# Kernel tuning notes

Hardware: AMD Instinct MI355X
Metric: run time of the kernel (lower is better)

## Reference

```python
import jax, jax.numpy as jnp
import numpy as np


def lrelu(x):
    return jnp.where(x > 0, x, 0.1 * x)


def setup_inputs() -> dict:
    key = jax.random.key(0)
    ks = jax.random.split(key, 16)
    L, B, E = 160, 16, 512
    C, H, DM, DO = 256, 512, 128, 512  # conv channels, enc_hid, d_mlp, dec_hid

    def rn(k, shape, scale=0.05):
        return jax.random.normal(k, shape, dtype=jnp.float32) * scale

    return {
        "x": rn(ks[0], (L, B, E), 1.0),
        "h": rn(ks[1], (B, H), 1.0),
        "conv_w": rn(ks[2], (C, E, 3)),
        "conv_b": rn(ks[3], (C,)),
        "bn_g": jnp.ones((C,), jnp.float32),
        "bn_b": jnp.zeros((C,), jnp.float32),
        "W1": rn(ks[4], (DM, 2 * (C + 2) + H)),
        "b1": rn(ks[5], (DM,)),
        "W2": rn(ks[6], (DM, DM)), "b2": rn(ks[7], (DM,)),
        "W3": rn(ks[8], (DM, DM)), "b3": rn(ks[9], (DM,)),
        "W4": rn(ks[10], (DM, DM)), "b4": rn(ks[11], (DM,)),
        "W5": rn(ks[12], (DM, DM)), "b5": rn(ks[13], (DM,)),
        "W6": rn(ks[14], (DO, DM)), "b6": rn(ks[15], (DO,)),
    }


def reference(x, h, conv_w, conv_b, bn_g, bn_b,
              W1, b1, W2, b2, W3, b3, W4, b4, W5, b5, W6, b6):
    L, B, E = x.shape
    # --- ConvLayer: Conv1d(k=3, pad=1) -> LeakyReLU(0.1) -> BatchNorm1d (training stats)
    xc = jnp.transpose(x, (1, 2, 0))  # (B, E, L)
    y = jax.lax.conv_general_dilated(xc, conv_w, (1,), [(1, 1)],
                                     dimension_numbers=("NCH", "OIH", "NCH"))
    y = lrelu(y + conv_b[None, :, None])
    mu = y.mean(axis=(0, 2), keepdims=True)
    var = y.var(axis=(0, 2), keepdims=True)  # biased variance (torch training BN)
    y = (y - mu) * jax.lax.rsqrt(var + 1e-5)
    y = y * bn_g[None, :, None] + bn_b[None, :, None]
    y = jnp.transpose(y, (0, 2, 1))  # (B, L, C)

    # --- coordinate features: [(i/sqrt(L)-2)/2, (i % sqrt(L) - 2)/2]
    sL = np.sqrt(L)
    i = jnp.arange(L, dtype=jnp.float32)
    coords = jnp.stack([(i / sL - 2.0) / 2.0, (jnp.mod(i, sL) - 2.0) / 2.0], axis=-1)  # (L, 2)
    xf = jnp.concatenate([y, jnp.broadcast_to(coords[None], (B, L, 2))], axis=-1)  # (B, L, C+2)
    Cp = xf.shape[-1]

    # --- g_mlp first Linear decomposed over [x_i | x_j | h] feature blocks:
    # x_i[b,a,c] = xf[b,c] (varies with dim2); x_j[b,a,c] = cat(xf[b,a], h[b]) (varies with dim1)
    W1i = W1[:, :Cp]            # acts on x_i
    W1jx = W1[:, Cp:2 * Cp]     # acts on x part of x_j
    W1jh = W1[:, 2 * Cp:]       # acts on h part of x_j
    u = jnp.einsum('blc,dc->bld', xf, W1i)                     # (B, L, DM), index = dim2
    v = jnp.einsum('blc,dc->bld', xf, W1jx) + (h @ W1jh.T)[:, None, :]  # (B, L, DM), index = dim1
    z = lrelu(v[:, :, None, :] + u[:, None, :, :] + b1)        # (B, L, L, DM)
    z = lrelu(z @ W2.T + b2)
    z = lrelu(z @ W3.T + b3)
    z = lrelu(z @ W4.T + b4)
    s = z.sum(axis=(1, 2))  # sum over all L*L pairs -> (B, DM)

    # --- f_mlp
    s = lrelu(s @ W5.T + b5)
    return lrelu(s @ W6.T + b6)  # (B, dec_hid)
```

## Files before the change

kernel.cpp:

```cpp
#include <hip/hip_runtime.h>
#include <cstdint>

typedef unsigned short u16;
typedef uint32_t u32;

typedef __bf16 bf16x8 __attribute__((ext_vector_type(8)));
typedef float  f32x2  __attribute__((ext_vector_type(2)));
typedef float  f32x4  __attribute__((ext_vector_type(4)));
typedef float  f32x16 __attribute__((ext_vector_type(16)));
typedef u16    u16x4  __attribute__((ext_vector_type(4)));
typedef u16    u16x8  __attribute__((ext_vector_type(8)));

__device__ __forceinline__ u16 f2bf(float f) {
    u32 x = __float_as_uint(f);
    return (u16)((x + 0x7FFFu + ((x >> 16) & 1u)) >> 16);
}
__device__ __forceinline__ float lrelu(float x) { return fmaxf(x, 0.1f * x); }

__device__ __forceinline__ u32 pack_rn(float lo, float hi) {
    u32 a = __float_as_uint(lo) + 0x8000u;
    u32 b = __float_as_uint(hi) + 0x8000u;
    return __builtin_amdgcn_perm(b, a, 0x07060302u);
}

__global__ __launch_bounds__(256) void k_prep(
    const float* __restrict__ x, const float* __restrict__ conv_w,
    const float* __restrict__ W2, const float* __restrict__ W3, const float* __restrict__ W4,
    const float* __restrict__ b2, const float* __restrict__ b3, const float* __restrict__ b4,
    const float* __restrict__ h, const float* __restrict__ W1,
    u16* __restrict__ xb, u16* __restrict__ wcb_f, u16* __restrict__ wfrag,
    u16* __restrict__ w1frag, float* __restrict__ hW, float* __restrict__ zero0)
{
    int blk = blockIdx.x, tid = threadIdx.x;
    if (blk < 1280) {
        int o = (blk * 256 + tid) * 4;
        int e = o & 511;
        int bl = o >> 9;
        int b = bl / 160, l = bl % 160;
        f32x4 v = *(const f32x4*)(x + ((size_t)(l * 16 + b)) * 512 + e);
        u16x4 ov;
        ov[0] = f2bf(v[0]); ov[1] = f2bf(v[1]); ov[2] = f2bf(v[2]); ov[3] = f2bf(v[3]);
        *(u16x4*)&xb[o] = ov;
    } else if (blk < 1472) {
        int g = (blk - 1280) * 256 + tid;
        int lane = g & 63;
        int ks = (g >> 6) % 48;
        int cb = g / 3072;
        int c = cb * 16 + (lane & 15);
        int quad = lane >> 4;
        int k0 = ks * 32 + quad * 8;
        int tap = k0 >> 9, e0 = k0 & 511;
        u16x8 ov;
        #pragma unroll
        for (int j = 0; j < 8; j++)
            ov[j] = f2bf(conv_w[((size_t)c * 512 + e0 + j) * 3 + tap]);
        *(u16x8*)&wcb_f[(size_t)g * 8] = ov;
    } else if (blk < 1526) {
        int o = ((blk - 1472) * 256 + tid) * 4;
        int layer = o / 18432, rem = o % 18432;
        int ks9 = rem >> 11;
        int rem2 = rem & 2047;
        int hh = rem2 >> 10;
        int rem3 = rem2 & 1023;
        int n = rem3 >> 3, j0 = rem3 & 7;
        const float* W = (layer == 0) ? W2 : (layer == 1) ? W3 : W4;
        const float* bi = (layer == 0) ? b2 : (layer == 1) ? b3 : b4;
        u16x4 ov;
        if (ks9 < 8) {
            f32x4 v = *(const f32x4*)(W + (size_t)n * 128 + 16 * ks9 + 8 * hh + j0);
            ov[0] = f2bf(v[0]); ov[1] = f2bf(v[1]); ov[2] = f2bf(v[2]); ov[3] = f2bf(v[3]);
        } else {
            ov[0] = (hh == 0 && j0 == 0) ? f2bf(bi[n]) : (u16)0;
            ov[1] = 0; ov[2] = 0; ov[3] = 0;
        }
        *(u16x4*)&wfrag[o] = ov;
    } else if (blk < 1598) {
        int o = ((blk - 1526) * 256 + tid) * 4;
        int nt = o / 4608;
        int rem = o % 4608;
        int ks = rem >> 9;
        int rem2 = rem & 511;
        int lane = rem2 >> 3, j0 = rem2 & 7;
        int n = nt * 16 + (lane & 15);
        int k0 = ks * 32 + (lane >> 4) * 8 + j0;
        const float* wr = (n < 128) ? (W1 + (size_t)n * 1028)
                                    : (W1 + (size_t)(n - 128) * 1028 + 258);
        u16x4 ov;
        #pragma unroll
        for (int q = 0; q < 4; q++) {
            int k = k0 + q;
            ov[q] = (k < 258) ? f2bf(wr[k]) : (u16)0;
        }
        *(u16x4*)&w1frag[o] = ov;
    } else if (blk < 1726) {
        int gid = (blk - 1598) * 256 + tid;
        int outp = gid >> 4, q = gid & 15;
        int b = outp >> 7, d = outp & 127;
        const float* hr = h + (size_t)b * 512;
        const float* wr = W1 + (size_t)d * 1028 + 516;
        float acc = 0.f;
        #pragma unroll
        for (int c = 0; c < 8; c++) {
            int k = c * 64 + q * 4;
            f32x4 hv = *(const f32x4*)(hr + k);
            f32x4 wv = *(const f32x4*)(wr + k);
            acc += hv[0]*wv[0] + hv[1]*wv[1] + hv[2]*wv[2] + hv[3]*wv[3];
        }
        acc += __shfl_xor(acc, 1); acc += __shfl_xor(acc, 2);
        acc += __shfl_xor(acc, 4); acc += __shfl_xor(acc, 8);
        if (q == 0) hW[outp] = acc;
    } else {
        int idx = (blk - 1726) * 256 + tid;
        if (idx < 640) {
            f32x4 z = {0.f, 0.f, 0.f, 0.f};
            *(f32x4*)&zero0[idx * 4] = z;
        }
    }
}

__global__ __launch_bounds__(256, 4) void k_conv(
    const u16* __restrict__ xb, const u16* __restrict__ wcb_f,
    const float* __restrict__ conv_b,
    float* __restrict__ ws_y, float* __restrict__ stats)
{
    __shared__ u16 xs[18 * 520];
    int tid = threadIdx.x, wg = blockIdx.x;
    int rowtile = wg >> 2, cg = wg & 3;
    int b = rowtile / 10, l0 = (rowtile % 10) * 16;

    for (int t = tid; t < 18 * 64; t += 256) {
        int s = t >> 6, ch = t & 63;
        int lg = l0 + s - 1;
        u16x8 v = {};
        if (lg >= 0 && lg < 160)
            v = *(const u16x8*)(xb + ((size_t)(b * 160 + lg)) * 512 + ch * 8);
        *(u16x8*)&xs[s * 520 + ch * 8] = v;
    }
    __syncthreads();

    int lane = tid & 63, w = tid >> 6;
    int row16 = lane & 15, quad = lane >> 4;
    int cb = cg * 4 + w;
    int c_n = cb * 16 + row16;
    const u16* wb = wcb_f + (size_t)cb * 24576;

    f32x4 acc0 = {0,0,0,0};
    for (int ks4 = 0; ks4 < 48; ks4 += 4) {
        bf16x8 wf[4];
        #pragma unroll
        for (int q = 0; q < 4; q++)
            wf[q] = *(const bf16x8*)(wb + (size_t)((ks4 + q) * 64 + lane) * 8);
        #pragma unroll
        for (int q = 0; q < 4; q++) {
            int k = (ks4 + q) * 32 + quad * 8;
            int tap = k >> 9, e = k & 511;
            bf16x8 a0 = *(const bf16x8*)&xs[(row16 + tap) * 520 + e];
            acc0 = __builtin_amdgcn_mfma_f32_16x16x32_bf16(a0, wf[q], acc0, 0, 0, 0);
        }
    }

    float bias = conv_b[c_n];
    float sum = 0.f, sq = 0.f;
    #pragma unroll
    for (int r = 0; r < 4; r++) {
        float v = lrelu(acc0[r] + bias);
        int lr = l0 + quad * 4 + r;
        ws_y[((size_t)(b * 160 + lr)) * 256 + c_n] = v;
        sum += v; sq += v * v;
    }
    sum += __shfl_xor(sum, 16); sum += __shfl_xor(sum, 32);
    sq  += __shfl_xor(sq, 16);  sq  += __shfl_xor(sq, 32);
    if (quad == 0) {
        atomicAdd(&stats[c_n], sum);
        atomicAdd(&stats[256 + c_n], sq);
    }
}

__global__ __launch_bounds__(256) void k_uv(
    const float* __restrict__ ws_y, const float* __restrict__ stats,
    const float* __restrict__ bn_g, const float* __restrict__ bn_b,
    const u16* __restrict__ w1frag, const float* __restrict__ b1,
    const float* __restrict__ hW,
    float* __restrict__ uu, float* __restrict__ vv)
{
    __shared__ float a_s[256], c_s[256];
    __shared__ __align__(16) u16 xfs[16 * 296];
    int tid = threadIdx.x;
    int row0 = blockIdx.x * 16;
    int b = row0 / 160, l0 = row0 % 160;
    {
        int c = tid;
        float mu  = stats[c] * (1.0f / 2560.0f);
        float var = stats[256 + c] * (1.0f / 2560.0f) - mu * mu;
        float rs  = rsqrtf(var + 1e-5f) * bn_g[c];
        a_s[c] = rs;
        c_s[c] = bn_b[c] - mu * rs;
    }
    __syncthreads();
    float sLf = sqrtf(160.0f);
    for (int idx = tid; idx < 16 * 288; idx += 256) {
        int r = idx / 288, c = idx - r * 288;
        int l = l0 + r;
        float v = 0.f;
        if (c < 256) {
            v = ws_y[((size_t)(b * 160 + l)) * 256 + c] * a_s[c] + c_s[c];
        } else if (c == 256) {
            v = ((float)l / sLf - 2.0f) * 0.5f;
        } else if (c == 257) {
            float fi = (float)l;
            float m = fi - floorf(fi / sLf) * sLf;
            v = (m - 2.0f) * 0.5f;
        }
        xfs[r * 296 + c] = f2bf(v);
    }
    __syncthreads();

    int lane = tid & 63, w = tid >> 6;
    int row16 = lane & 15, quad = lane >> 4;

    bf16x8 af[9];
    #pragma unroll
    for (int ks = 0; ks < 9; ks++)
        af[ks] = *(const bf16x8*)&xfs[row16 * 296 + ks * 32 + quad * 8];

    f32x4 acc[4];
    #pragma unroll
    for (int nt = 0; nt < 4; nt++) {
        f32x4 a = {0.f, 0.f, 0.f, 0.f};
        #pragma unroll
        for (int ks = 0; ks < 9; ks++) {
            bf16x8 bf = *(const bf16x8*)(w1frag +
                (size_t)(((w * 4 + nt) * 9 + ks) * 64 + lane) * 8);
            a = __builtin_amdgcn_mfma_f32_16x16x32_bf16(af[ks], bf, a, 0, 0, 0);
        }
        acc[nt] = a;
    }

    #pragma unroll
    for (int nt = 0; nt < 4; nt++) {
        int n = (w * 4 + nt) * 16 + row16;
        bool isv = n >= 128;
        int d = n & 127;
        float add = isv ? (hW[b * 128 + d] + b1[d]) : 0.f;
        float* dst = isv ? vv : uu;
        #pragma unroll
        for (int r = 0; r < 4; r++) {
            int l = l0 + quad * 4 + r;
            dst[((size_t)(b * 160 + l)) * 128 + d] = acc[nt][r] + add;
        }
    }
}

__global__ __launch_bounds__(256, 4) void k_mlp(
    const float* __restrict__ vv, const float* __restrict__ uu,
    const u16* __restrict__ wfrag,
    float* __restrict__ s_glob)
{
    __shared__ __align__(16) u16 Wlds[18432];
    __shared__ float spart[128];
    int tid = threadIdx.x;
    int wave = tid >> 6, lane = tid & 63;
    int h = lane >> 5, lo = lane & 31;
    int b = blockIdx.x / 200, sub = blockIdx.x % 200;
    int tileb = sub * 4 + wave;

    if (tid < 128) spart[tid] = 0.f;

    u32 selv = h ? 0x07060302u : 0x05040100u;
    uint4 biasfrag;
    biasfrag.x = (h == 0) ? 0x00003F80u : 0u;
    biasfrag.y = 0u; biasfrag.z = 0u; biasfrag.w = 0u;

    f32x16 Z;
    #pragma unroll
    for (int r = 0; r < 16; r++) Z[r] = 0.f;

    uint4 B[8], Bn[8];
    float ssum[4];

    int i  = (tileb / 10) * 2  + (lo >> 4);
    int jj = (tileb % 10) * 16 + (lo & 15);
    const float* vr = vv + ((size_t)(b * 160 + i))  * 128 + 8 * h;
    const float* ur = uu + ((size_t)(b * 160 + jj)) * 128 + 8 * h;

    for (int layer = 0; layer < 3; layer++) {
        __syncthreads();
        {
            const uint4* src = (const uint4*)(wfrag + layer * 18432);
            #pragma unroll
            for (int it = 0; it < 9; it++) {
                int idx = it * 256 + tid;
                *(uint4*)&Wlds[idx * 8] = src[idx];
            }
        }
        __syncthreads();

        if (layer == 0) {
            #pragma unroll
            for (int ks = 0; ks < 8; ks++) {
                f32x4 v0 = *(const f32x4*)(vr + 16 * ks);
                f32x4 v1 = *(const f32x4*)(vr + 16 * ks + 4);
                f32x4 u0 = *(const f32x4*)(ur + 16 * ks);
                f32x4 u1 = *(const f32x4*)(ur + 16 * ks + 4);
                uint4 d;
                d.x = pack_rn(lrelu(v0[0]+u0[0]), lrelu(v0[1]+u0[1]));
                d.y = pack_rn(lrelu(v0[2]+u0[2]), lrelu(v0[3]+u0[3]));
                d.z = pack_rn(lrelu(v1[0]+u1[0]), lrelu(v1[1]+u1[1]));
                d.w = pack_rn(lrelu(v1[2]+u1[2]), lrelu(v1[3]+u1[3]));
                B[ks] = d;
            }
        }

        #pragma unroll
        for (int nt = 0; nt < 4; nt++) {
            f32x16 a;
            #pragma unroll
            for (int ks = 0; ks < 9; ks++) {
                bf16x8 wf = *(const bf16x8*)&Wlds[(size_t)(ks * 256 + h * 128 + nt * 32 + lo) * 8];
                uint4 zu = (ks < 8) ? B[ks] : biasfrag;
                bf16x8 zf = *(bf16x8*)&zu;
                if (layer < 2)
                    a = __builtin_amdgcn_mfma_f32_32x32x16_bf16(wf, zf, ks ? a : Z, 0, 0, 0);
                else
                    a = __builtin_amdgcn_mfma_f32_32x32x16_bf16(zf, wf, ks ? a : Z, 0, 0, 0);
            }

            if (layer < 2) {
                u32 own[4][2], oth[4][2];
                #pragma unroll
                for (int c = 0; c < 4; c++)
                    #pragma unroll
                    for (int p = 0; p < 2; p++)
                        own[c][p] = pack_rn(lrelu(a[c + 8*p]),
                                            lrelu(a[c + 4 + 8*p]));
                #pragma unroll
                for (int c = 0; c < 4; c++)
                    #pragma unroll
                    for (int p = 0; p < 2; p++)
                        oth[c][p] = (u32)__shfl_xor((int)own[c][p], 32);
                #pragma unroll
                for (int p = 0; p < 2; p++) {
                    u32 dA0 = __builtin_amdgcn_perm(own[1][p], own[0][p], selv);
                    u32 dB0 = __builtin_amdgcn_perm(oth[1][p], oth[0][p], selv);
                    u32 dA1 = __builtin_amdgcn_perm(own[3][p], own[2][p], selv);
                    u32 dB1 = __builtin_amdgcn_perm(oth[3][p], oth[2][p], selv);
                    uint4 d;
                    d.x = h ? dB0 : dA0;
                    d.y = h ? dB1 : dA1;
                    d.z = h ? dA0 : dB0;
                    d.w = h ? dA1 : dB1;
                    Bn[2 * nt + p] = d;
                }
            } else {
                float t = 0.f;
                #pragma unroll
                for (int r = 0; r < 16; r++)
                    t += lrelu(a[r]);
                ssum[nt] = t;
            }
        }

        if (layer < 2) {
            #pragma unroll
            for (int ks = 0; ks < 8; ks++) B[ks] = Bn[ks];
        }
    }

    #pragma unroll
    for (int nt = 0; nt < 4; nt++) {
        float v = ssum[nt] + __shfl_xor(ssum[nt], 32);
        if (h == 0) atomicAdd(&spart[nt * 32 + lo], v);
    }
    __syncthreads();
    if (tid < 128) atomicAdd(&s_glob[b * 128 + tid], spart[tid]);
}

__global__ __launch_bounds__(256) void k_final(
    const float* __restrict__ s_glob,
    const float* __restrict__ W5, const float* __restrict__ b5,
    const float* __restrict__ W6, const float* __restrict__ b6,
    float* __restrict__ out)
{
    __shared__ float sh[128], t5[128];
    int b = blockIdx.x, tid = threadIdx.x;
    if (tid < 128) sh[tid] = s_glob[b * 128 + tid];
    __syncthreads();
    if (tid < 128) {
        const float* wr = W5 + (size_t)tid * 128;
        float acc = b5[tid];
        #pragma unroll
        for (int k = 0; k < 128; k += 4) {
            f32x4 wv = *(const f32x4*)(wr + k);
            f32x4 sv = *(const f32x4*)&sh[k];
            acc += wv[0]*sv[0] + wv[1]*sv[1] + wv[2]*sv[2] + wv[3]*sv[3];
        }
        t5[tid] = lrelu(acc);
    }
    __syncthreads();
    #pragma unroll
    for (int q = 0; q < 2; q++) {
        int o = q * 256 + tid;
        const float* wr = W6 + (size_t)o * 128;
        float acc = b6[o];
        #pragma unroll
        for (int k = 0; k < 128; k += 4) {
            f32x4 wv = *(const f32x4*)(wr + k);
            f32x4 tv = *(const f32x4*)&t5[k];
            acc += wv[0]*tv[0] + wv[1]*tv[1] + wv[2]*tv[2] + wv[3]*tv[3];
        }
        out[b * 512 + o] = lrelu(acc);
    }
}

extern "C" void kernel_launch(void* const* d_in, const int* in_sizes, int n_in,
                              void* d_out, int out_size, void* d_ws, size_t ws_size,
                              hipStream_t stream)
{
    const float* x      = (const float*)d_in[0];
    const float* h      = (const float*)d_in[1];
    const float* conv_w = (const float*)d_in[2];
    const float* conv_b = (const float*)d_in[3];
    const float* bn_g   = (const float*)d_in[4];
    const float* bn_b   = (const float*)d_in[5];
    const float* W1     = (const float*)d_in[6];
    const float* b1     = (const float*)d_in[7];
    const float* W2     = (const float*)d_in[8];
    const float* b2     = (const float*)d_in[9];
    const float* W3     = (const float*)d_in[10];
    const float* b3     = (const float*)d_in[11];
    const float* W4     = (const float*)d_in[12];
    const float* b4     = (const float*)d_in[13];
    const float* W5     = (const float*)d_in[14];
    const float* b5     = (const float*)d_in[15];
    const float* W6     = (const float*)d_in[16];
    const float* b6     = (const float*)d_in[17];

    char* ws = (char*)d_ws;
    float* s_glob = (float*)(ws + 0);
    float* stats  = (float*)(ws + 8192);
    float* hW     = (float*)(ws + 10240);
    float* ws_y   = (float*)(ws + 18432);
    float* vv     = (float*)(ws + 2639872);
    float* uu     = (float*)(ws + 3950592);
    u16*   xb     = (u16*)  (ws + 5261312);
    u16*   wcb_f  = (u16*)  (ws + 7882752);
    u16*   wfrag  = (u16*)  (ws + 8669184);
    u16*   w1frag = (u16*)  (ws + 8779776);

    k_prep <<<1729, 256, 0, stream>>>(x, conv_w, W2, W3, W4, b2, b3, b4, h, W1,
                                      xb, wcb_f, wfrag, w1frag, hW, s_glob);
    k_conv <<<640, 256, 0, stream>>>(xb, wcb_f, conv_b, ws_y, stats);
    k_uv   <<<160, 256, 0, stream>>>(ws_y, stats, bn_g, bn_b, w1frag, b1, hW, uu, vv);
    k_mlp  <<<3200, 256, 0, stream>>>(vv, uu, wfrag, s_glob);
    k_final<<<16, 256, 0, stream>>>(s_glob, W5, b5, W6, b6, (float*)d_out);
}
```

Baseline: 193.2 us.

## Fuse all stages into one cooperative persistent kernel with grid syncs

Replaces the five separate launches with a single cooperative kernel that loops over each stage's work units and separates stages with grid-wide syncs, keeping a multi-launch fallback. This removes per-launch overhead and inter-kernel gaps. In exchange the grid is capped at occupancy × 256 CUs (max 800), so the 3200 MLP units run as a persistent loop. All stages now share one 37 KB LDS allocation and register budget, which may lower occupancy for the lighter stages, and the grid barriers add their own cost.

Measured after the change: 731.4 us. 279% more time.

```diff
diff --git a/kernel.cpp b/kernel.cpp
--- a/kernel.cpp
+++ b/kernel.cpp
@@ -1,5 +1,8 @@
 #include <hip/hip_runtime.h>
+#include <hip/hip_cooperative_groups.h>
 #include <cstdint>
+
+namespace cg = cooperative_groups;
 
 typedef unsigned short u16;
 typedef uint32_t u32;
@@ -23,15 +26,14 @@
     return __builtin_amdgcn_perm(b, a, 0x07060302u);
 }
 
-__global__ __launch_bounds__(256) void k_prep(
-    const float* __restrict__ x, const float* __restrict__ conv_w,
-    const float* __restrict__ W2, const float* __restrict__ W3, const float* __restrict__ W4,
-    const float* __restrict__ b2, const float* __restrict__ b3, const float* __restrict__ b4,
-    const float* __restrict__ h, const float* __restrict__ W1,
-    u16* __restrict__ xb, u16* __restrict__ wcb_f, u16* __restrict__ wfrag,
-    u16* __restrict__ w1frag, float* __restrict__ hW, float* __restrict__ zero0)
-{
-    int blk = blockIdx.x, tid = threadIdx.x;
+__device__ __forceinline__ void prep_block(int blk, int tid,
+    const float* x, const float* conv_w,
+    const float* W2, const float* W3, const float* W4,
+    const float* b2, const float* b3, const float* b4,
+    const float* h, const float* W1,
+    u16* xb, u16* wcb_f, u16* wfrag, u16* w1frag,
+    float* hW, float* zero0)
+{
     if (blk < 1280) {
         int o = (blk * 256 + tid) * 4;
         int e = o & 511;
@@ -118,14 +120,11 @@
     }
 }
 
-__global__ __launch_bounds__(256, 4) void k_conv(
-    const u16* __restrict__ xb, const u16* __restrict__ wcb_f,
-    const float* __restrict__ conv_b,
-    float* __restrict__ ws_y, float* __restrict__ stats)
-{
-    __shared__ u16 xs[18 * 520];
-    int tid = threadIdx.x, wg = blockIdx.x;
-    int rowtile = wg >> 2, cg = wg & 3;
+__device__ __forceinline__ void conv_block(int wg, int tid, u16* xs,
+    const u16* xb, const u16* wcb_f, const float* conv_b,
+    float* ws_y, float* stats)
+{
+    int rowtile = wg >> 2, cgp = wg & 3;
     int b = rowtile / 10, l0 = (rowtile % 10) * 16;
 
     for (int t = tid; t < 18 * 64; t += 256) {
@@ -140,7 +139,7 @@
 
     int lane = tid & 63, w = tid >> 6;
     int row16 = lane & 15, quad = lane >> 4;
-    int cb = cg * 4 + w;
+    int cb = cgp * 4 + w;
     int c_n = cb * 16 + row16;
     const u16* wb = wcb_f + (size_t)cb * 24576;
 
@@ -174,19 +173,19 @@
         atomicAdd(&stats[c_n], sum);
         atomicAdd(&stats[256 + c_n], sq);
     }
-}
-
-__global__ __launch_bounds__(256) void k_uv(
-    const float* __restrict__ ws_y, const float* __restrict__ stats,
-    const float* __restrict__ bn_g, const float* __restrict__ bn_b,
-    const u16* __restrict__ w1frag, const float* __restrict__ b1,
-    const float* __restrict__ hW,
-    float* __restrict__ uu, float* __restrict__ vv)
-{
-    __shared__ float a_s[256], c_s[256];
-    __shared__ __align__(16) u16 xfs[16 * 296];
-    int tid = threadIdx.x;
-    int row0 = blockIdx.x * 16;
+    __syncthreads();
+}
+
+__device__ __forceinline__ void uv_block(int wg, int tid, unsigned char* smem,
+    const float* ws_y, const float* stats,
+    const float* bn_g, const float* bn_b,
+    const u16* w1frag, const float* b1, const float* hW,
+    float* uu, float* vv)
+{
+    float* a_s = (float*)smem;
+    float* c_s = (float*)(smem + 1024);
+    u16*   xfs = (u16*)(smem + 2048);
+    int row0 = wg * 16;
     int b = row0 / 160, l0 = row0 % 160;
     {
         int c = tid;
@@ -223,7 +222,6 @@
     for (int ks = 0; ks < 9; ks++)
         af[ks] = *(const bf16x8*)&xfs[row16 * 296 + ks * 32 + quad * 8];
 
-    f32x4 acc[4];
     #pragma unroll
     for (int nt = 0; nt < 4; nt++) {
         f32x4 a = {0.f, 0.f, 0.f, 0.f};
@@ -233,11 +231,6 @@
                 (size_t)(((w * 4 + nt) * 9 + ks) * 64 + lane) * 8);
             a = __builtin_amdgcn_mfma_f32_16x16x32_bf16(af[ks], bf, a, 0, 0, 0);
         }
-        acc[nt] = a;
-    }
-
-    #pragma unroll
-    for (int nt = 0; nt < 4; nt++) {
         int n = (w * 4 + nt) * 16 + row16;
         bool isv = n >= 128;
         int d = n & 127;
@@ -246,22 +239,18 @@
         #pragma unroll
         for (int r = 0; r < 4; r++) {
             int l = l0 + quad * 4 + r;
-            dst[((size_t)(b * 160 + l)) * 128 + d] = acc[nt][r] + add;
-        }
-    }
-}
-
-__global__ __launch_bounds__(256, 4) void k_mlp(
-    const float* __restrict__ vv, const float* __restrict__ uu,
-    const u16* __restrict__ wfrag,
-    float* __restrict__ s_glob)
-{
-    __shared__ __align__(16) u16 Wlds[18432];
-    __shared__ float spart[128];
-    int tid = threadIdx.x;
+            dst[((size_t)(b * 160 + l)) * 128 + d] = a[r] + add;
+        }
+    }
+}
+
+__device__ __forceinline__ void mlp_unit(int unit, int tid,
+    u16* Wlds, float* spart,
+    const float* vv, const float* uu, const u16* wfrag, float* s_glob)
+{
     int wave = tid >> 6, lane = tid & 63;
     int h = lane >> 5, lo = lane & 31;
-    int b = blockIdx.x / 200, sub = blockIdx.x % 200;
+    int b = unit / 200, sub = unit % 200;
     int tileb = sub * 4 + wave;
 
     if (tid < 128) spart[tid] = 0.f;
@@ -375,14 +364,14 @@
     if (tid < 128) atomicAdd(&s_glob[b * 128 + tid], spart[tid]);
 }
 
-__global__ __launch_bounds__(256) void k_final(
-    const float* __restrict__ s_glob,
-    const float* __restrict__ W5, const float* __restrict__ b5,
-    const float* __restrict__ W6, const float* __restrict__ b6,
-    float* __restrict__ out)
-{
-    __shared__ float sh[128], t5[128];
-    int b = blockIdx.x, tid = threadIdx.x;
+__device__ __forceinline__ void final_block(int b, int tid, unsigned char* smem,
+    const float* s_glob,
+    const float* W5, const float* b5,
+    const float* W6, const float* b6,
+    float* out)
+{
+    float* sh = (float*)smem;
+    float* t5 = (float*)(smem + 512);
     if (tid < 128) sh[tid] = s_glob[b * 128 + tid];
     __syncthreads();
     if (tid < 128) {
@@ -410,6 +399,109 @@
         }
         out[b * 512 + o] = lrelu(acc);
     }
+}
+
+__global__ __launch_bounds__(256, 4) void k_all(
+    const float* __restrict__ x, const float* __restrict__ h,
+    const float* __restrict__ conv_w, const float* __restrict__ conv_b,
+    const float* __restrict__ bn_g, const float* __restrict__ bn_b,
+    const float* __restrict__ W1, const float* __restrict__ b1,
+    const float* __restrict__ W2, const float* __restrict__ b2,
+    const float* __restrict__ W3, const float* __restrict__ b3,
+    const float* __restrict__ W4, const float* __restrict__ b4,
+    const float* __restrict__ W5, const float* __restrict__ b5,
+    const float* __restrict__ W6, const float* __restrict__ b6,
+    float* __restrict__ out, char* __restrict__ ws)
+{
+    __shared__ __align__(16) unsigned char smem[37376];
+    int tid = threadIdx.x, wg = blockIdx.x, gdim = gridDim.x;
+    cg::grid_group grid = cg::this_grid();
+
+    float* s_glob = (float*)(ws);
+    float* stats  = (float*)(ws + 8192);
+    float* hW     = (float*)(ws + 10240);
+    float* ws_y   = (float*)(ws + 18432);
+    float* vv     = (float*)(ws + 2639872);
+    float* uu     = (float*)(ws + 3950592);
+    u16*   xb     = (u16*)  (ws + 5261312);
+    u16*   wcb_f  = (u16*)  (ws + 7882752);
+    u16*   wfrag  = (u16*)  (ws + 8669184);
+    u16*   w1frag = (u16*)  (ws + 8779776);
+
+    for (int g = wg; g < 1729; g += gdim)
+        prep_block(g, tid, x, conv_w, W2, W3, W4, b2, b3, b4, h, W1,
+                   xb, wcb_f, wfrag, w1frag, hW, s_glob);
+    __threadfence();
+    grid.sync();
+
+    for (int u = wg; u < 640; u += gdim)
+        conv_block(u, tid, (u16*)smem, xb, wcb_f, conv_b, ws_y, stats);
+    __threadfence();
+    grid.sync();
+
+    for (int u = wg; u < 160; u += gdim)
+        uv_block(u, tid, smem, ws_y, stats, bn_g, bn_b, w1frag, b1, hW, uu, vv);
+    __threadfence();
+    grid.sync();
+
+    {
+        u16*   Wlds  = (u16*)smem;
+        float* spart = (float*)(smem + 36864);
+        #pragma unroll 1
+        for (int u = wg; u < 3200; u += gdim)
+            mlp_unit(u, tid, Wlds, spart, vv, uu, wfrag, s_glob);
+    }
+    __threadfence();
+    grid.sync();
+
+    for (int u = wg; u < 16; u += gdim)
+        final_block(u, tid, smem, s_glob, W5, b5, W6, b6, out);
+}
+
+__global__ __launch_bounds__(256) void k_prep_g(
+    const float* x, const float* conv_w,
+    const float* W2, const float* W3, const float* W4,
+    const float* b2, const float* b3, const float* b4,
+    const float* h, const float* W1,
+    u16* xb, u16* wcb_f, u16* wfrag, u16* w1frag, float* hW, float* zero0)
+{
+    prep_block(blockIdx.x, threadIdx.x, x, conv_w, W2, W3, W4, b2, b3, b4,
+               h, W1, xb, wcb_f, wfrag, w1frag, hW, zero0);
+}
+
+__global__ __launch_bounds__(256, 4) void k_conv_g(
+    const u16* xb, const u16* wcb_f, const float* conv_b,
+    float* ws_y, float* stats)
+{
+    __shared__ u16 xs[18 * 520];
+    conv_block(blockIdx.x, threadIdx.x, xs, xb, wcb_f, conv_b, ws_y, stats);
+}
+
+__global__ __launch_bounds__(256) void k_uv_g(
+    const float* ws_y, const float* stats,
+    const float* bn_g, const float* bn_b,
+    const u16* w1frag, const float* b1, const float* hW,
+    float* uu, float* vv)
+{
+    __shared__ __align__(16) unsigned char smem[2048 + 16 * 296 * 2];
+    uv_block(blockIdx.x, threadIdx.x, smem, ws_y, stats, bn_g, bn_b,
+             w1frag, b1, hW, uu, vv);
+}
+
+__global__ __launch_bounds__(256, 4) void k_mlp_g(
+    const float* vv, const float* uu, const u16* wfrag, float* s_glob)
+{
+    __shared__ __align__(16) u16 Wlds[18432];
+    __shared__ float spart[128];
+    mlp_unit(blockIdx.x, threadIdx.x, Wlds, spart, vv, uu, wfrag, s_glob);
+}
+
+__global__ __launch_bounds__(256) void k_final_g(
+    const float* s_glob, const float* W5, const float* b5,
+    const float* W6, const float* b6, float* out)
+{
+    __shared__ __align__(16) unsigned char smem[1024];
+    final_block(blockIdx.x, threadIdx.x, smem, s_glob, W5, b5, W6, b6, out);
 }
 
 extern "C" void kernel_launch(void* const* d_in, const int* in_sizes, int n_in,
@@ -434,9 +526,10 @@
     const float* b5     = (const float*)d_in[15];
     const float* W6     = (const float*)d_in[16];
     const float* b6     = (const float*)d_in[17];
-
-    char* ws = (char*)d_ws;
-    float* s_glob = (float*)(ws + 0);
+    float* out = (float*)d_out;
+    char*  ws  = (char*)d_ws;
+
+    float* s_glob = (float*)(ws);
     float* stats  = (float*)(ws + 8192);
     float* hW     = (float*)(ws + 10240);
     float* ws_y   = (float*)(ws + 18432);
@@ -447,10 +540,31 @@
     u16*   wfrag  = (u16*)  (ws + 8669184);
     u16*   w1frag = (u16*)  (ws + 8779776);
 
-    k_prep <<<1729, 256, 0, stream>>>(x, conv_w, W2, W3, W4, b2, b3, b4, h, W1,
-                                      xb, wcb_f, wfrag, w1frag, hW, s_glob);
-    k_conv <<<640, 256, 0, stream>>>(xb, wcb_f, conv_b, ws_y, stats);
-    k_uv   <<<160, 256, 0, stream>>>(ws_y, stats, bn_g, bn_b, w1frag, b1, hW, uu, vv);
-    k_mlp  <<<3200, 256, 0, stream>>>(vv, uu, wfrag, s_glob);
-    k_final<<<16, 256, 0, stream>>>(s_glob, W5, b5, W6, b6, (float*)d_out);
-}
+    int occ = 0;
+    hipError_t qerr = hipOccupancyMaxActiveBlocksPerMultiprocessor(&occ, k_all, 256, 0);
+    int grid = (qerr == hipSuccess && occ > 0) ? occ * 256 : 0;
+    if (grid > 800) grid = 800;
+
+    bool done = false;
+    if (grid >= 256) {
+        void* params[] = {
+            (void*)&x, (void*)&h, (void*)&conv_w, (void*)&conv_b,
+            (void*)&bn_g, (void*)&bn_b, (void*)&W1, (void*)&b1,
+            (void*)&W2, (void*)&b2, (void*)&W3, (void*)&b3,
+            (void*)&W4, (void*)&b4, (void*)&W5, (void*)&b5,
+            (void*)&W6, (void*)&b6, (void*)&out, (void*)&ws
+        };
+        hipError_t lerr = hipLaunchCooperativeKernel(k_all, dim3(grid), dim3(256),
+                                                     params, 0, stream);
+        done = (lerr == hipSuccess);
+    }
+
+    if (!done) {
+        k_prep_g <<<1729, 256, 0, stream>>>(x, conv_w, W2, W3, W4, b2, b3, b4,
+                                            h, W1, xb, wcb_f, wfrag, w1frag, hW, s_glob);
+        k_conv_g <<<640, 256, 0, stream>>>(xb, wcb_f, conv_b, ws_y, stats);
+        k_uv_g   <<<160, 256, 0, stream>>>(ws_y, stats, bn_g, bn_b, w1frag, b1, hW, uu, vv);
+        k_mlp_g  <<<3200, 256, 0, stream>>>(vv, uu, wfrag, s_glob);
+        k_final_g<<<16, 256, 0, stream>>>(s_glob, W5, b5, W6, b6, out);
+    }
+}
```

## Fuse x bf16 conversion into conv load and final MLP into last mlp block

Applied to the files above, without the earlier changes.

The separate fp32-to-bf16 pass over x in the prep kernel is removed. The conv kernel now reads fp32 x directly and converts while filling shared memory, which drops one round trip through the workspace. The k_final launch is removed: the last k_mlp block, found through an atomic completion counter, computes the f_mlp for all 16 batches. This saves a launch, but the final stage now runs serially in a single block, and correctness depends on fences and the counter reset in k_prep.

Result: slower. 381.1 us (+97.3%).

```diff
diff --git a/kernel.cpp b/kernel.cpp
--- a/kernel.cpp
+++ b/kernel.cpp
@@ -5,7 +5,6 @@
 typedef uint32_t u32;
 
 typedef __bf16 bf16x8 __attribute__((ext_vector_type(8)));
-typedef float  f32x2  __attribute__((ext_vector_type(2)));
 typedef float  f32x4  __attribute__((ext_vector_type(4)));
 typedef float  f32x16 __attribute__((ext_vector_type(16)));
 typedef u16    u16x4  __attribute__((ext_vector_type(4)));
@@ -24,25 +23,16 @@
 }
 
 __global__ __launch_bounds__(256) void k_prep(
-    const float* __restrict__ x, const float* __restrict__ conv_w,
+    const float* __restrict__ conv_w,
     const float* __restrict__ W2, const float* __restrict__ W3, const float* __restrict__ W4,
     const float* __restrict__ b2, const float* __restrict__ b3, const float* __restrict__ b4,
     const float* __restrict__ h, const float* __restrict__ W1,
-    u16* __restrict__ xb, u16* __restrict__ wcb_f, u16* __restrict__ wfrag,
-    u16* __restrict__ w1frag, float* __restrict__ hW, float* __restrict__ zero0)
+    u16* __restrict__ wcb_f, u16* __restrict__ wfrag, u16* __restrict__ w1frag,
+    float* __restrict__ hW, float* __restrict__ zero0, u32* __restrict__ ctr)
 {
     int blk = blockIdx.x, tid = threadIdx.x;
-    if (blk < 1280) {
-        int o = (blk * 256 + tid) * 4;
-        int e = o & 511;
-        int bl = o >> 9;
-        int b = bl / 160, l = bl % 160;
-        f32x4 v = *(const f32x4*)(x + ((size_t)(l * 16 + b)) * 512 + e);
-        u16x4 ov;
-        ov[0] = f2bf(v[0]); ov[1] = f2bf(v[1]); ov[2] = f2bf(v[2]); ov[3] = f2bf(v[3]);
-        *(u16x4*)&xb[o] = ov;
-    } else if (blk < 1472) {
-        int g = (blk - 1280) * 256 + tid;
+    if (blk < 192) {
+        int g = blk * 256 + tid;
         int lane = g & 63;
         int ks = (g >> 6) % 48;
         int cb = g / 3072;
@@ -55,8 +45,8 @@
         for (int j = 0; j < 8; j++)
             ov[j] = f2bf(conv_w[((size_t)c * 512 + e0 + j) * 3 + tap]);
         *(u16x8*)&wcb_f[(size_t)g * 8] = ov;
-    } else if (blk < 1526) {
-        int o = ((blk - 1472) * 256 + tid) * 4;
+    } else if (blk < 246) {
+        int o = ((blk - 192) * 256 + tid) * 4;
         int layer = o / 18432, rem = o % 18432;
         int ks9 = rem >> 11;
         int rem2 = rem & 2047;
@@ -74,8 +64,8 @@
             ov[1] = 0; ov[2] = 0; ov[3] = 0;
         }
         *(u16x4*)&wfrag[o] = ov;
-    } else if (blk < 1598) {
-        int o = ((blk - 1526) * 256 + tid) * 4;
+    } else if (blk < 318) {
+        int o = ((blk - 246) * 256 + tid) * 4;
         int nt = o / 4608;
         int rem = o % 4608;
         int ks = rem >> 9;
@@ -92,8 +82,8 @@
             ov[q] = (k < 258) ? f2bf(wr[k]) : (u16)0;
         }
         *(u16x4*)&w1frag[o] = ov;
-    } else if (blk < 1726) {
-        int gid = (blk - 1598) * 256 + tid;
+    } else if (blk < 446) {
+        int gid = (blk - 318) * 256 + tid;
         int outp = gid >> 4, q = gid & 15;
         int b = outp >> 7, d = outp & 127;
         const float* hr = h + (size_t)b * 512;
@@ -110,37 +100,45 @@
         acc += __shfl_xor(acc, 4); acc += __shfl_xor(acc, 8);
         if (q == 0) hW[outp] = acc;
     } else {
-        int idx = (blk - 1726) * 256 + tid;
+        int idx = (blk - 446) * 256 + tid;
         if (idx < 640) {
             f32x4 z = {0.f, 0.f, 0.f, 0.f};
             *(f32x4*)&zero0[idx * 4] = z;
         }
+        if (idx == 0) *ctr = 0u;
     }
 }
 
 __global__ __launch_bounds__(256, 4) void k_conv(
-    const u16* __restrict__ xb, const u16* __restrict__ wcb_f,
+    const float* __restrict__ x, const u16* __restrict__ wcb_f,
     const float* __restrict__ conv_b,
     float* __restrict__ ws_y, float* __restrict__ stats)
 {
     __shared__ u16 xs[18 * 520];
     int tid = threadIdx.x, wg = blockIdx.x;
-    int rowtile = wg >> 2, cg = wg & 3;
+    int rowtile = wg >> 2, cgp = wg & 3;
     int b = rowtile / 10, l0 = (rowtile % 10) * 16;
 
     for (int t = tid; t < 18 * 64; t += 256) {
         int s = t >> 6, ch = t & 63;
         int lg = l0 + s - 1;
-        u16x8 v = {};
-        if (lg >= 0 && lg < 160)
-            v = *(const u16x8*)(xb + ((size_t)(b * 160 + lg)) * 512 + ch * 8);
-        *(u16x8*)&xs[s * 520 + ch * 8] = v;
+        u16x8 ov = {};
+        if (lg >= 0 && lg < 160) {
+            const float* src = x + ((size_t)(lg * 16 + b)) * 512 + ch * 8;
+            f32x4 v0 = *(const f32x4*)src;
+            f32x4 v1 = *(const f32x4*)(src + 4);
+            ov[0] = f2bf(v0[0]); ov[1] = f2bf(v0[1]);
+            ov[2] = f2bf(v0[2]); ov[3] = f2bf(v0[3]);
+            ov[4] = f2bf(v1[0]); ov[5] = f2bf(v1[1]);
+            ov[6] = f2bf(v1[2]); ov[7] = f2bf(v1[3]);
+        }
+        *(u16x8*)&xs[s * 520 + ch * 8] = ov;
     }
     __syncthreads();
 
     int lane = tid & 63, w = tid >> 6;
     int row16 = lane & 15, quad = lane >> 4;
-    int cb = cg * 4 + w;
+    int cb = cgp * 4 + w;
     int c_n = cb * 16 + row16;
     const u16* wb = wcb_f + (size_t)cb * 24576;
 
@@ -223,7 +221,6 @@
     for (int ks = 0; ks < 9; ks++)
         af[ks] = *(const bf16x8*)&xfs[row16 * 296 + ks * 32 + quad * 8];
 
-    f32x4 acc[4];
     #pragma unroll
     for (int nt = 0; nt < 4; nt++) {
         f32x4 a = {0.f, 0.f, 0.f, 0.f};
@@ -233,11 +230,6 @@
                 (size_t)(((w * 4 + nt) * 9 + ks) * 64 + lane) * 8);
             a = __builtin_amdgcn_mfma_f32_16x16x32_bf16(af[ks], bf, a, 0, 0, 0);
         }
-        acc[nt] = a;
-    }
-
-    #pragma unroll
-    for (int nt = 0; nt < 4; nt++) {
         int n = (w * 4 + nt) * 16 + row16;
         bool isv = n >= 128;
         int d = n & 127;
@@ -246,7 +238,7 @@
         #pragma unroll
         for (int r = 0; r < 4; r++) {
             int l = l0 + quad * 4 + r;
-            dst[((size_t)(b * 160 + l)) * 128 + d] = acc[nt][r] + add;
+            dst[((size_t)(b * 160 + l)) * 128 + d] = a[r] + add;
         }
     }
 }
@@ -254,10 +246,15 @@
 __global__ __launch_bounds__(256, 4) void k_mlp(
     const float* __restrict__ vv, const float* __restrict__ uu,
     const u16* __restrict__ wfrag,
-    float* __restrict__ s_glob)
+    float* __restrict__ s_glob, u32* __restrict__ ctr,
+    const float* __restrict__ W5, const float* __restrict__ b5,
+    const float* __restrict__ W6, const float* __restrict__ b6,
+    float* __restrict__ out)
 {
     __shared__ __align__(16) u16 Wlds[18432];
     __shared__ float spart[128];
+    __shared__ float fin[256];
+    __shared__ bool lastflag;
     int tid = threadIdx.x;
     int wave = tid >> 6, lane = tid & 63;
     int h = lane >> 5, lo = lane & 31;
@@ -373,42 +370,50 @@
     }
     __syncthreads();
     if (tid < 128) atomicAdd(&s_glob[b * 128 + tid], spart[tid]);
-}
-
-__global__ __launch_bounds__(256) void k_final(
-    const float* __restrict__ s_glob,
-    const float* __restrict__ W5, const float* __restrict__ b5,
-    const float* __restrict__ W6, const float* __restrict__ b6,
-    float* __restrict__ out)
-{
-    __shared__ float sh[128], t5[128];
-    int b = blockIdx.x, tid = threadIdx.x;
-    if (tid < 128) sh[tid] = s_glob[b * 128 + tid];
-    __syncthreads();
-    if (tid < 128) {
-        const float* wr = W5 + (size_t)tid * 128;
-        float acc = b5[tid];
-        #pragma unroll
-        for (int k = 0; k < 128; k += 4) {
-            f32x4 wv = *(const f32x4*)(wr + k);
-            f32x4 sv = *(const f32x4*)&sh[k];
-            acc += wv[0]*sv[0] + wv[1]*sv[1] + wv[2]*sv[2] + wv[3]*sv[3];
-        }
-        t5[tid] = lrelu(acc);
-    }
-    __syncthreads();
-    #pragma unroll
-    for (int q = 0; q < 2; q++) {
-        int o = q * 256 + tid;
-        const float* wr = W6 + (size_t)o * 128;
-        float acc = b6[o];
-        #pragma unroll
-        for (int k = 0; k < 128; k += 4) {
-            f32x4 wv = *(const f32x4*)(wr + k);
-            f32x4 tv = *(const f32x4*)&t5[k];
-            acc += wv[0]*tv[0] + wv[1]*tv[1] + wv[2]*tv[2] + wv[3]*tv[3];
-        }
-        out[b * 512 + o] = lrelu(acc);
+
+    __syncthreads();
+    if (tid == 0) {
+        __threadfence();
+        u32 prev = atomicAdd(ctr, 1u);
+        lastflag = (prev == 3199u);
+    }
+    __syncthreads();
+    if (!lastflag) return;
+    __threadfence();
+
+    float* sh = fin;
+    float* t5 = fin + 128;
+    for (int bb = 0; bb < 16; bb++) {
+        if (tid < 128)
+            sh[tid] = __hip_atomic_load(&s_glob[bb * 128 + tid],
+                                        __ATOMIC_RELAXED, __HIP_MEMORY_SCOPE_AGENT);
+        __syncthreads();
+        if (tid < 128) {
+            const float* wr = W5 + (size_t)tid * 128;
+            float acc = b5[tid];
+            #pragma unroll
+            for (int k = 0; k < 128; k += 4) {
+                f32x4 wv = *(const f32x4*)(wr + k);
+                f32x4 sv = *(const f32x4*)&sh[k];
+                acc += wv[0]*sv[0] + wv[1]*sv[1] + wv[2]*sv[2] + wv[3]*sv[3];
+            }
+            t5[tid] = lrelu(acc);
+        }
+        __syncthreads();
+        #pragma unroll
+        for (int q = 0; q < 2; q++) {
+            int o = q * 256 + tid;
+            const float* wr = W6 + (size_t)o * 128;
+            float acc = b6[o];
+            #pragma unroll
+            for (int k = 0; k < 128; k += 4) {
+                f32x4 wv = *(const f32x4*)(wr + k);
+                f32x4 tv = *(const f32x4*)&t5[k];
+                acc += wv[0]*tv[0] + wv[1]*tv[1] + wv[2]*tv[2] + wv[3]*tv[3];
+            }
+            out[bb * 512 + o] = lrelu(acc);
+        }
+        __syncthreads();
     }
 }
 
@@ -434,23 +439,24 @@
     const float* b5     = (const float*)d_in[15];
     const float* W6     = (const float*)d_in[16];
     const float* b6     = (const float*)d_in[17];
-
-    char* ws = (char*)d_ws;
-    float* s_glob = (float*)(ws + 0);
+    float* out = (float*)d_out;
+    char*  ws  = (char*)d_ws;
+
+    float* s_glob = (float*)(ws);
     float* stats  = (float*)(ws + 8192);
     float* hW     = (float*)(ws + 10240);
     float* ws_y   = (float*)(ws + 18432);
     float* vv     = (float*)(ws + 2639872);
     float* uu     = (float*)(ws + 3950592);
-    u16*   xb     = (u16*)  (ws + 5261312);
     u16*   wcb_f  = (u16*)  (ws + 7882752);
     u16*   wfrag  = (u16*)  (ws + 8669184);
     u16*   w1frag = (u16*)  (ws + 8779776);
-
-    k_prep <<<1729, 256, 0, stream>>>(x, conv_w, W2, W3, W4, b2, b3, b4, h, W1,
-                                      xb, wcb_f, wfrag, w1frag, hW, s_glob);
-    k_conv <<<640, 256, 0, stream>>>(xb, wcb_f, conv_b, ws_y, stats);
+    u32*   ctr    = (u32*)  (ws + 8927232);
+
+    k_prep <<<449, 256, 0, stream>>>(conv_w, W2, W3, W4, b2, b3, b4, h, W1,
+                                     wcb_f, wfrag, w1frag, hW, s_glob, ctr);
+    k_conv <<<640, 256, 0, stream>>>(x, wcb_f, conv_b, ws_y, stats);
     k_uv   <<<160, 256, 0, stream>>>(ws_y, stats, bn_g, bn_b, w1frag, b1, hW, uu, vv);
-    k_mlp  <<<3200, 256, 0, stream>>>(vv, uu, wfrag, s_glob);
-    k_final<<<16, 256, 0, stream>>>(s_glob, W5, b5, W6, b6, (float*)d_out);
-}
+    k_mlp  <<<3200, 256, 0, stream>>>(vv, uu, wfrag, s_glob, ctr,
+                                      W5, b5, W6, b6, out);
+}
```
